# Kernel optimization log

Measured on AMD Instinct MI355X. Metric: run time of the kernel, lower is better.

## Reference

```python
import jax, jax.numpy as jnp
import numpy as np

# Complete 32-ary tree of depth 3: vocab = 32**3 = 32768 leaves.
B = 4096       # batch
NHID = 512     # hidden size
BR = 32        # branching factor (num_children at every internal node)
DEPTH = 3      # number of internal-node decisions from root to leaf
V = BR ** DEPTH
NUM_NODES = sum(BR ** k for k in range(DEPTH))  # 1 + 32 + 1024 = 1057

# Static tree-indexing tables (level-order node numbering).
_LEVEL_OFFSET = np.array([sum(BR ** j for j in range(k)) for k in range(DEPTH)], dtype=np.int64)   # [0, 1, 33]
_NODE_DIV = np.array([BR ** (DEPTH - k) for k in range(DEPTH)], dtype=np.int64)                    # node-within-level divisor
_STEP_DIV = np.array([BR ** (DEPTH - 1 - k) for k in range(DEPTH)], dtype=np.int64)                # child-step divisor


def setup_inputs() -> dict:
    key = jax.random.key(0)
    k1, k2, k3 = jax.random.split(key, 3)
    inputs = jax.random.normal(k1, (B, NHID), dtype=jnp.float32)
    labels = jax.random.randint(k2, (B,), 0, V)                     # leaf index per sample
    W = jax.random.normal(k3, (NUM_NODES, NHID, BR), dtype=jnp.float32)  # all node params, stacked
    return {"inputs": inputs, "labels": labels, "W": W}


def reference(inputs, labels, W):
    lab = labels[:, None]                                            # [B, 1]
    node_idx = jnp.asarray(_LEVEL_OFFSET)[None, :] + lab // jnp.asarray(_NODE_DIV)[None, :]  # [B, D] node on path
    steps = (lab // jnp.asarray(_STEP_DIV)[None, :]) % BR            # [B, D] child taken at each node
    Wg = W[node_idx]                                                 # [B, D, NHID, BR] gathered path params
    logits = jnp.einsum('bh,bdhc->bdc', inputs, Wg)                  # [B, D, BR]
    p = jax.nn.softmax(logits, axis=-1)
    step_p = jnp.take_along_axis(p, steps[:, :, None], axis=-1)[..., 0]  # [B, D]
    return jnp.prod(step_p, axis=-1)                                 # [B] path probability
```

## Files before the change

kernel.cpp:

```cpp
#include <hip/hip_runtime.h>


#define NHID  512
#define BR    32
#define BATCH 4096
#define NBUCK 1024
#define SMAX  8
#define GMAX  1536

#define FMA4(A, xv, wv_) do { \
    (A).x = fmaf((xv), (wv_).x, (A).x); \
    (A).y = fmaf((xv), (wv_).y, (A).y); \
    (A).z = fmaf((xv), (wv_).z, (A).z); \
    (A).w = fmaf((xv), (wv_).w, (A).w); } while (0)

__device__ __forceinline__ void dma16(const float* g, float* l) {
    __builtin_amdgcn_global_load_lds(
        (const __attribute__((address_space(1))) void*)g,
        (__attribute__((address_space(3))) void*)l,
        16, 0, 0);
}
__device__ __forceinline__ void wait_vm4() {
    asm volatile("s_waitcnt vmcnt(4)" ::: "memory");
}
__device__ __forceinline__ void wait_vm0() {
    asm volatile("s_waitcnt vmcnt(0)" ::: "memory");
}

__global__ __launch_bounds__(1024) void k_sort(const int* __restrict__ labels,
                                               int* __restrict__ order,
                                               int* __restrict__ ngroups,
                                               int* __restrict__ gdesc) {
    __shared__ int labs[BATCH];
    __shared__ int hist[NBUCK];
    __shared__ int wsum1[16];
    __shared__ int wsum2[16];
    const int t  = threadIdx.x;
    const int wv = t >> 6;
    const int ln = t & 63;

    hist[t] = 0;
    #pragma unroll
    for (int r = 0; r < BATCH / 1024; ++r)
        labs[t + 1024 * r] = labels[t + 1024 * r];
    __syncthreads();
    #pragma unroll
    for (int r = 0; r < BATCH / 1024; ++r)
        atomicAdd(&hist[labs[t + 1024 * r] >> 5], 1);
    __syncthreads();

    const int cnt  = hist[t];
    const int gcnt = (cnt + SMAX - 1) / SMAX;

    int s1 = cnt, s2 = gcnt;
    #pragma unroll
    for (int d = 1; d < 64; d <<= 1) {
        int u1 = __shfl_up(s1, d);
        int u2 = __shfl_up(s2, d);
        if (ln >= d) { s1 += u1; s2 += u2; }
    }
    if (ln == 63) { wsum1[wv] = s1; wsum2[wv] = s2; }
    __syncthreads();
    if (t < 16) {
        int a = wsum1[t], b = wsum2[t];
        #pragma unroll
        for (int d = 1; d < 16; d <<= 1) {
            int ua = __shfl_up(a, d, 16);
            int ub = __shfl_up(b, d, 16);
            if (t >= d) { a += ua; b += ub; }
        }
        wsum1[t] = a; wsum2[t] = b;
        if (t == 15) *ngroups = b;
    }
    __syncthreads();
    const int base1 = (wv > 0) ? wsum1[wv - 1] : 0;
    const int base2 = (wv > 0) ? wsum2[wv - 1] : 0;
    const int off  = base1 + s1 - cnt;
    const int goff = base2 + s2 - gcnt;
    hist[t] = off;
    __syncthreads();

    for (int j = 0; j < gcnt; ++j)
        gdesc[goff + j] = (off + j * SMAX)
                        | (min(SMAX, cnt - j * SMAX) << 12)
                        | (t << 16);

    #pragma unroll
    for (int r = 0; r < BATCH / 1024; ++r) {
        int j = t + 1024 * r;
        int pos = atomicAdd(&hist[labs[j] >> 5], 1);
        order[pos] = j;
    }
}

__global__ __launch_bounds__(192) void hsm_dma(
    const float* __restrict__ inputs,
    const int* __restrict__ labels,
    const float* __restrict__ W,
    const int* __restrict__ order,
    const int* __restrict__ ngroups,
    const int* __restrict__ gdesc,
    float* __restrict__ out)
{
    __shared__ float xsT[NHID * SMAX];
    __shared__ float wlds[3 * 2 * 1024];
    __shared__ float pk[3][SMAX];
    __shared__ int   sids[SMAX];
    __shared__ int   slab[SMAX];

    const int gid = blockIdx.x;
    if (gid >= *ngroups) return;
    const int d     = gdesc[gid];
    const int start = d & 0xFFF;
    const int m     = (d >> 12) & 0xF;
    const int g     = d >> 16;
    const int tid   = threadIdx.x;

    if (tid < SMAX) {
        int sid = (tid < m) ? order[start + tid] : -1;
        sids[tid] = sid;
        slab[tid] = (sid >= 0) ? labels[sid] : 0;
    }
    __syncthreads();

    for (int h = tid; h < NHID; h += 192) {
        float v[SMAX];
        #pragma unroll
        for (int s = 0; s < SMAX; ++s) {
            int id = sids[s];
            v[s] = (id >= 0) ? inputs[(size_t)id * NHID + h] : 0.0f;
        }
        float4* dst = (float4*)&xsT[h * SMAX];
        dst[0] = make_float4(v[0], v[1], v[2], v[3]);
        dst[1] = make_float4(v[4], v[5], v[6], v[7]);
    }
    __syncthreads();

    const int wv   = tid >> 6;
    const int lane = tid & 63;
    const int colg = lane & 7;
    const int hsel = lane >> 3;

    const int node = (wv == 0) ? 0 : (wv == 1) ? 1 + (g >> 5) : 33 + g;
    const int step01 = (wv == 0) ? (g >> 5) : (g & 31);

    const float* wg = W + (size_t)node * (NHID * BR);
    float* wb = &wlds[wv * 2048];

    float4 acc[SMAX];
    #pragma unroll
    for (int s = 0; s < SMAX; ++s) acc[s] = make_float4(0, 0, 0, 0);

    #pragma unroll
    for (int j = 0; j < 4; ++j)
        dma16(wg + j * 256 + lane * 4, wb + j * 256);

    #pragma unroll 4
    for (int c = 0; c < 16; ++c) {
        const float* cur = wb + (c & 1) * 1024;
        float* nxt = wb + ((c + 1) & 1) * 1024;
        if (c < 15) {
            const float* gsrc = wg + (c + 1) * 1024;
            #pragma unroll
            for (int j = 0; j < 4; ++j)
                dma16(gsrc + j * 256 + lane * 4, nxt + j * 256);
            wait_vm4();
        } else {
            wait_vm0();
        }
        #pragma unroll
        for (int t = 0; t < 4; ++t) {
            const int rr = hsel + 8 * t;
            float4 w = *(const float4*)&cur[rr * 32 + colg * 4];
            const float4* xr = (const float4*)&xsT[(c * 32 + rr) * SMAX];
            float4 xa = xr[0];
            float4 xb = xr[1];
            FMA4(acc[0], xa.x, w); FMA4(acc[1], xa.y, w);
            FMA4(acc[2], xa.z, w); FMA4(acc[3], xa.w, w);
            FMA4(acc[4], xb.x, w); FMA4(acc[5], xb.y, w);
            FMA4(acc[6], xb.z, w); FMA4(acc[7], xb.w, w);
        }
    }

    #pragma unroll
    for (int s = 0; s < SMAX; ++s) {
        #pragma unroll
        for (int mm = 8; mm <= 32; mm <<= 1) {
            acc[s].x += __shfl_xor(acc[s].x, mm);
            acc[s].y += __shfl_xor(acc[s].y, mm);
            acc[s].z += __shfl_xor(acc[s].z, mm);
            acc[s].w += __shfl_xor(acc[s].w, mm);
        }
    }

    #pragma unroll
    for (int s = 0; s < SMAX; ++s) {
        float4 a = acc[s];
        float mx = fmaxf(fmaxf(a.x, a.y), fmaxf(a.z, a.w));
        #pragma unroll
        for (int mm = 1; mm <= 4; mm <<= 1) mx = fmaxf(mx, __shfl_xor(mx, mm));
        float es = expf(a.x - mx) + expf(a.y - mx) + expf(a.z - mx) + expf(a.w - mx);
        #pragma unroll
        for (int mm = 1; mm <= 4; mm <<= 1) es += __shfl_xor(es, mm);

        int step = (wv == 2) ? (slab[s] & 31) : step01;
        int e = step & 3;
        float v = (e == 0) ? a.x : (e == 1) ? a.y : (e == 2) ? a.z : a.w;
        float sl = __shfl(v, step >> 2);
        float p = expf(sl - mx) / es;
        if (lane == 0) pk[wv][s] = p;
    }
    __syncthreads();

    if (tid < SMAX && sids[tid] >= 0)
        out[sids[tid]] = pk[0][tid] * pk[1][tid] * pk[2][tid];
}

extern "C" void kernel_launch(void* const* d_in, const int* in_sizes, int n_in,
                              void* d_out, int out_size, void* d_ws, size_t ws_size,
                              hipStream_t stream)
{
    const float* inputs = (const float*)d_in[0];
    const int*   labels = (const int*)d_in[1];
    const float* W      = (const float*)d_in[2];
    float* out = (float*)d_out;

    char* ws = (char*)d_ws;
    int* order   = (int*)ws;
    int* ngroups = (int*)(ws + 16384);
    int* gdesc   = (int*)(ws + 16384 + 128);

    k_sort <<<dim3(1),    dim3(1024), 0, stream>>>(labels, order, ngroups, gdesc);
    hsm_dma<<<dim3(GMAX), dim3(192),  0, stream>>>(inputs, labels, W, order,
                                                   ngroups, gdesc, out);
}
```

Measured before the change: 140.8 us.

## Triple-buffer weight DMA with prefetch depth two and swizzle LDS layout

```diff
diff --git a/kernel.cpp b/kernel.cpp
--- a/kernel.cpp
+++ b/kernel.cpp
@@ -20,12 +20,9 @@
         (__attribute__((address_space(3))) void*)l,
         16, 0, 0);
 }
-__device__ __forceinline__ void wait_vm4() {
-    asm volatile("s_waitcnt vmcnt(4)" ::: "memory");
-}
-__device__ __forceinline__ void wait_vm0() {
-    asm volatile("s_waitcnt vmcnt(0)" ::: "memory");
-}
+__device__ __forceinline__ void wait_vm8() { asm volatile("s_waitcnt vmcnt(8)" ::: "memory"); }
+__device__ __forceinline__ void wait_vm4() { asm volatile("s_waitcnt vmcnt(4)" ::: "memory"); }
+__device__ __forceinline__ void wait_vm0() { asm volatile("s_waitcnt vmcnt(0)" ::: "memory"); }
 
 __global__ __launch_bounds__(1024) void k_sort(const int* __restrict__ labels,
                                                int* __restrict__ order,
@@ -93,7 +90,7 @@
     }
 }
 
-__global__ __launch_bounds__(192) void hsm_dma(
+__global__ __launch_bounds__(192) void hsm_dma2(
     const float* __restrict__ inputs,
     const int* __restrict__ labels,
     const float* __restrict__ W,
@@ -103,7 +100,7 @@
     float* __restrict__ out)
 {
     __shared__ float xsT[NHID * SMAX];
-    __shared__ float wlds[3 * 2 * 1024];
+    __shared__ float wlds[3 * 3 * 1024];
     __shared__ float pk[3][SMAX];
     __shared__ int   sids[SMAX];
     __shared__ int   slab[SMAX];
@@ -144,34 +141,40 @@
     const int node = (wv == 0) ? 0 : (wv == 1) ? 1 + (g >> 5) : 33 + g;
     const int step01 = (wv == 0) ? (g >> 5) : (g & 31);
 
+    const int srcswz = (((lane & 7) + (lane >> 3)) & 7);
+    const int srcoff = (lane >> 3) * 32 + srcswz * 4;
     const float* wg = W + (size_t)node * (NHID * BR);
-    float* wb = &wlds[wv * 2048];
+    float* wb = &wlds[wv * 3072];
+    const int rdslot = ((colg + 8 - hsel) & 7) * 4;
 
     float4 acc[SMAX];
     #pragma unroll
     for (int s = 0; s < SMAX; ++s) acc[s] = make_float4(0, 0, 0, 0);
 
     #pragma unroll
-    for (int j = 0; j < 4; ++j)
-        dma16(wg + j * 256 + lane * 4, wb + j * 256);
-
-    #pragma unroll 4
+    for (int c = 0; c < 2; ++c)
+        #pragma unroll
+        for (int j = 0; j < 4; ++j)
+            dma16(wg + c * 1024 + j * 256 + srcoff, wb + (c % 3) * 1024 + j * 256);
+
+    #pragma unroll
     for (int c = 0; c < 16; ++c) {
-        const float* cur = wb + (c & 1) * 1024;
-        float* nxt = wb + ((c + 1) & 1) * 1024;
-        if (c < 15) {
-            const float* gsrc = wg + (c + 1) * 1024;
+        if (c + 2 < 16) {
+            const float* gsrc = wg + (c + 2) * 1024;
+            float* nxt = wb + ((c + 2) % 3) * 1024;
             #pragma unroll
             for (int j = 0; j < 4; ++j)
-                dma16(gsrc + j * 256 + lane * 4, nxt + j * 256);
-            wait_vm4();
-        } else {
-            wait_vm0();
-        }
+                dma16(gsrc + j * 256 + srcoff, nxt + j * 256);
+        }
+        if (c < 14)      wait_vm8();
+        else if (c == 14) wait_vm4();
+        else              wait_vm0();
+
+        const float* cur = wb + (c % 3) * 1024;
         #pragma unroll
         for (int t = 0; t < 4; ++t) {
             const int rr = hsel + 8 * t;
-            float4 w = *(const float4*)&cur[rr * 32 + colg * 4];
+            float4 w = *(const float4*)&cur[rr * 32 + rdslot];
             const float4* xr = (const float4*)&xsT[(c * 32 + rr) * SMAX];
             float4 xa = xr[0];
             float4 xb = xr[1];
@@ -230,7 +233,7 @@
     int* ngroups = (int*)(ws + 16384);
     int* gdesc   = (int*)(ws + 16384 + 128);
 
-    k_sort <<<dim3(1),    dim3(1024), 0, stream>>>(labels, order, ngroups, gdesc);
-    hsm_dma<<<dim3(GMAX), dim3(192),  0, stream>>>(inputs, labels, W, order,
-                                                   ngroups, gdesc, out);
-}
+    k_sort  <<<dim3(1),    dim3(1024), 0, stream>>>(labels, order, ngroups, gdesc);
+    hsm_dma2<<<dim3(GMAX), dim3(192),  0, stream>>>(inputs, labels, W, order,
+                                                    ngroups, gdesc, out);
+}
```

New measurement: 138.3 us. No clear change (-1.8%).
